# Kernel tuning notes

Measured on AMD Instinct MI355X. Metric: run time of the kernel, lower is better.

## Reference

```python
import jax, jax.numpy as jnp
import numpy as np

B, T, C, H, L, V = 4, 1024, 768, 12, 6, 32000
DH = C // H
EPS = 1e-5

def _ln(x, g, b):
    m = jnp.mean(x, axis=-1, keepdims=True)
    v = jnp.var(x, axis=-1, keepdims=True)
    return (x - m) * jax.lax.rsqrt(v + EPS) * g + b

def setup_inputs() -> dict:
    key = jax.random.key(0)
    ks = jax.random.split(key, 16)
    std = 0.02
    d = {
        'idx': jax.random.randint(ks[0], (B, T), 0, V),
        'tok_emb': jax.random.normal(ks[1], (V, C)) * std,
        'pos_emb': jnp.zeros((1, T, C)) + jax.random.normal(ks[2], (1, T, C)) * 0.01,
        'Wq': jax.random.normal(ks[3], (L, C, C)) * std, 'bq': jnp.zeros((L, C)),
        'Wk': jax.random.normal(ks[4], (L, C, C)) * std, 'bk': jnp.zeros((L, C)),
        'Wv': jax.random.normal(ks[5], (L, C, C)) * std, 'bv': jnp.zeros((L, C)),
        'Wo': jax.random.normal(ks[6], (L, C, C)) * std, 'bo': jnp.zeros((L, C)),
        'ln1_g': jnp.ones((L, C)), 'ln1_b': jnp.zeros((L, C)),
        'ln2_g': jnp.ones((L, C)), 'ln2_b': jnp.zeros((L, C)),
        'W1': jax.random.normal(ks[7], (L, C, 4 * C)) * std, 'b1': jnp.zeros((L, 4 * C)),
        'W2': jax.random.normal(ks[8], (L, 4 * C, C)) * std, 'b2': jnp.zeros((L, C)),
        'lnf_g': jnp.ones((C,)), 'lnf_b': jnp.zeros((C,)),
        'Whead': jax.random.normal(ks[9], (C, V)) * std,
    }
    return d

def _forward(idx, tok_emb, pos_emb, Wq, bq, Wk, bk, Wv, bv, Wo, bo,
             ln1_g, ln1_b, ln2_g, ln2_b, W1, b1, W2, b2, lnf_g, lnf_b, Whead):
    # pad-key mask: keys equal to vocab_size-1 are masked out (same for all queries)
    key_ok = (idx != V - 1)  # [B,T]
    x = tok_emb[idx] + pos_emb[:, :T, :]  # [B,T,C]
    for l in range(L):
        h = _ln(x, ln1_g[l], ln1_b[l])
        q = (h @ Wq[l] + bq[l]).reshape(B, T, H, DH)
        k = (h @ Wk[l] + bk[l]).reshape(B, T, H, DH)
        v = (h @ Wv[l] + bv[l]).reshape(B, T, H, DH)
        att = jnp.einsum('bqhd,bkhd->bhqk', q, k) * (1.0 / np.sqrt(DH))
        att = jnp.where(key_ok[:, None, None, :], att, -jnp.inf)
        att = jax.nn.softmax(att, axis=-1)
        y = jnp.einsum('bhqk,bkhd->bqhd', att, v).reshape(B, T, C)
        x = x + (y @ Wo[l] + bo[l])
        h2 = _ln(x, ln2_g[l], ln2_b[l])
        x = x + (jax.nn.gelu(h2 @ W1[l] + b1[l], approximate=False) @ W2[l] + b2[l])
    x = _ln(x, lnf_g, lnf_b)
    logits = x @ Whead  # [B,T,V]
    return logits

def reference(idx, tok_emb, pos_emb, Wq, bq, Wk, bk, Wv, bv, Wo, bo,
              ln1_g, ln1_b, ln2_g, ln2_b, W1, b1, W2, b2, lnf_g, lnf_b, Whead):
    logits = _forward(idx, tok_emb, pos_emb, Wq, bq, Wk, bk, Wv, bv, Wo, bo,
                      ln1_g, ln1_b, ln2_g, ln2_b, W1, b1, W2, b2, lnf_g, lnf_b, Whead)
    logsoftmax_logits = jax.nn.log_softmax(logits, axis=-1)
    softmax_logits = jax.nn.softmax(logits, axis=-1)
    seq_new_q = jnp.max(softmax_logits, axis=-1)
    seq_new = jnp.argmax(softmax_logits, axis=-1)
    return (seq_new, seq_new_q, logsoftmax_logits)
```

## Files before the change

kernel.cpp:

```cpp
#include <hip/hip_runtime.h>
#include <stdint.h>


#define B_ 4
#define T_ 1024
#define C_ 768
#define H_ 12
#define L_ 6
#define V_ 32000
#define CQ_ 2304
#define F_ 3072

typedef _Float16 f16;
typedef _Float16 f16x4 __attribute__((ext_vector_type(4)));
typedef _Float16 f16x8 __attribute__((ext_vector_type(8)));
typedef float f32x4 __attribute__((ext_vector_type(4)));

__device__ __forceinline__ f32x4 mfma16(f16x8 a, f16x8 b, f32x4 c) {
  return __builtin_amdgcn_mfma_f32_16x16x32_f16(a, b, c, 0, 0, 0);
}

__device__ __forceinline__ void gl_lds16(const void* g, void* l) {
  __builtin_amdgcn_global_load_lds((const __attribute__((address_space(1))) void*)g,
                                   (__attribute__((address_space(3))) void*)l, 16, 0, 0);
}

__global__ __launch_bounds__(256) void k_tsplit(const float* __restrict__ src,
    f16* __restrict__ dh, f16* __restrict__ dl, int K, int N,
    long long sS, long long dS)
{
  __shared__ float tile[64][68];
  src += (size_t)blockIdx.z * sS;
  dh += (size_t)blockIdx.z * dS;
  dl += (size_t)blockIdx.z * dS;
  const int t = threadIdx.x, tx = t & 15, ty = t >> 4;
  const int k0 = blockIdx.y * 64, n0 = blockIdx.x * 64;
#pragma unroll
  for (int rr = 0; rr < 4; rr++) {
    int row = ty + rr * 16;
    *(float4*)(&tile[row][tx * 4]) = *(const float4*)(src + (size_t)(k0 + row) * N + n0 + tx * 4);
  }
  __syncthreads();
#pragma unroll
  for (int rr = 0; rr < 4; rr++) {
    int nr = ty + rr * 16;
    f16x4 vh, vl;
#pragma unroll
    for (int j = 0; j < 4; j++) {
      float v = tile[tx * 4 + j][nr];
      f16 hv = (f16)v;
      vh[j] = hv;
      vl[j] = (f16)(v - (float)hv);
    }
    size_t o = (size_t)(n0 + nr) * K + k0 + tx * 4;
    *(f16x4*)(dh + o) = vh;
    *(f16x4*)(dl + o) = vl;
  }
}

__global__ __launch_bounds__(256) void k_bqkv(const float* __restrict__ bq, const float* __restrict__ bk,
    const float* __restrict__ bv, float* __restrict__ dst)
{
  int g = blockIdx.x * 256 + threadIdx.x;
  int lr = g / CQ_, j = g - lr * CQ_;
  float v;
  if (j < 768) v = bq[lr * 768 + j];
  else if (j < 1536) v = bk[lr * 768 + j - 768];
  else v = bv[lr * 768 + j - 1536];
  dst[g] = v;
}

__global__ __launch_bounds__(256) void k_embed(const int* __restrict__ idx, const float* __restrict__ tok,
    const float* __restrict__ pos, float* __restrict__ x)
{
  int g = blockIdx.x * 256 + threadIdx.x;
  int e = g * 4;
  int bt = e / C_;
  int c = e - bt * C_;
  int tt = bt & (T_ - 1);
  float4 a = *(const float4*)(tok + (size_t)idx[bt] * C_ + c);
  float4 p = *(const float4*)(pos + (size_t)tt * C_ + c);
  float4 o = {a.x + p.x, a.y + p.y, a.z + p.z, a.w + p.w};
  *(float4*)(x + e) = o;
}

__global__ __launch_bounds__(256) void k_ln(const float* __restrict__ x, const float* __restrict__ gg,
    const float* __restrict__ bb, f16* __restrict__ oh, f16* __restrict__ ol)
{
  __shared__ float red0[256], red1[256];
  const int row = blockIdx.x, t = threadIdx.x;
  const float* xr = x + (size_t)row * C_;
  float v0 = xr[t], v1 = xr[t + 256], v2 = xr[t + 512];
  red0[t] = v0 + v1 + v2;
  red1[t] = v0 * v0 + v1 * v1 + v2 * v2;
  __syncthreads();
  for (int off = 128; off > 0; off >>= 1) {
    if (t < off) { red0[t] += red0[t + off]; red1[t] += red1[t + off]; }
    __syncthreads();
  }
  const float mean = red0[0] * (1.f / C_);
  const float var = red1[0] * (1.f / C_) - mean * mean;
  const float rstd = rsqrtf(var + 1e-5f);
  const size_t o = (size_t)row * C_;
  float vv[3] = {v0, v1, v2};
#pragma unroll
  for (int i = 0; i < 3; i++) {
    int c = t + i * 256;
    float hv = (vv[i] - mean) * rstd * gg[c] + bb[c];
    f16 hh = (f16)hv;
    oh[o + c] = hh;
    ol[o + c] = (f16)(hv - (float)hh);
  }
}

template<int EPI>
__global__ __launch_bounds__(256, 2) void k_gemm(
    const f16* __restrict__ Ah, const f16* __restrict__ Al,
    const f16* __restrict__ Bh, const f16* __restrict__ Bl,
    const float* __restrict__ bias, const float* __restrict__ resid,
    float* __restrict__ outf, f16* __restrict__ outh, f16* __restrict__ outl,
    int M, int N, int K)
{
  __shared__ f16 sAh[128 * 32], sAl[128 * 32], sBh[128 * 32], sBl[128 * 32];
  const int t = threadIdx.x;
  const int l = t & 63, l15 = l & 15, quad = l >> 4;
  const int w = t >> 6;
  const int wm = (w >> 1) * 64, wn = (w & 1) * 64;
  const int m0 = blockIdx.y * 128, n0 = blockIdx.x * 128;
  const int r0 = t >> 2;
  const int c8 = (t & 3) * 8;

  f32x4 acc[4][4];
#pragma unroll
  for (int i = 0; i < 4; i++)
#pragma unroll
    for (int j = 0; j < 4; j++) acc[i][j] = (f32x4){0.f, 0.f, 0.f, 0.f};

  for (int k0 = 0; k0 < K; k0 += 32) {
    __syncthreads();
    const size_t ga0 = (size_t)(m0 + r0) * K + k0 + c8;
    const size_t ga1 = (size_t)(m0 + 64 + r0) * K + k0 + c8;
    const size_t gb0 = (size_t)(n0 + r0) * K + k0 + c8;
    const size_t gb1 = (size_t)(n0 + 64 + r0) * K + k0 + c8;
    gl_lds16(Ah + ga0, sAh + (size_t)t * 8);
    gl_lds16(Ah + ga1, sAh + (size_t)(256 + t) * 8);
    gl_lds16(Al + ga0, sAl + (size_t)t * 8);
    gl_lds16(Al + ga1, sAl + (size_t)(256 + t) * 8);
    gl_lds16(Bh + gb0, sBh + (size_t)t * 8);
    gl_lds16(Bh + gb1, sBh + (size_t)(256 + t) * 8);
    gl_lds16(Bl + gb0, sBl + (size_t)t * 8);
    gl_lds16(Bl + gb1, sBl + (size_t)(256 + t) * 8);
    __syncthreads();
    f16x8 fah[4], fal[4], fbh[4], fbl[4];
#pragma unroll
    for (int i = 0; i < 4; i++) {
      int ra = (wm + i * 16 + l15) * 32 + quad * 8;
      fah[i] = *(const f16x8*)(sAh + ra);
      fal[i] = *(const f16x8*)(sAl + ra);
    }
#pragma unroll
    for (int j = 0; j < 4; j++) {
      int rb = (wn + j * 16 + l15) * 32 + quad * 8;
      fbh[j] = *(const f16x8*)(sBh + rb);
      fbl[j] = *(const f16x8*)(sBl + rb);
    }
#pragma unroll
    for (int i = 0; i < 4; i++)
#pragma unroll
      for (int j = 0; j < 4; j++) {
        acc[i][j] = mfma16(fal[i], fbh[j], acc[i][j]);
        acc[i][j] = mfma16(fah[i], fbl[j], acc[i][j]);
        acc[i][j] = mfma16(fah[i], fbh[j], acc[i][j]);
      }
  }

#pragma unroll
  for (int j = 0; j < 4; j++) {
    int col = n0 + wn + j * 16 + l15;
    float bv = 0.f;
    if constexpr (EPI != 3) bv = bias[col];
#pragma unroll
    for (int i = 0; i < 4; i++) {
      int rowb = m0 + wm + i * 16 + quad * 4;
#pragma unroll
      for (int r = 0; r < 4; r++) {
        size_t o = (size_t)(rowb + r) * N + col;
        float v = acc[i][j][r] + bv;
        if constexpr (EPI == 1) v = 0.5f * v * (1.f + erff(v * 0.70710678118f));
        if constexpr (EPI == 0 || EPI == 1) {
          f16 hv = (f16)v;
          outh[o] = hv;
          outl[o] = (f16)(v - (float)hv);
        } else if constexpr (EPI == 2) {
          outf[o] = resid[o] + v;
        } else {
          outf[o] = v;
        }
      }
    }
  }
}

__global__ __launch_bounds__(256, 2) void k_attn(
    const f16* __restrict__ qh, const f16* __restrict__ ql,
    const int* __restrict__ idx, f16* __restrict__ yh, f16* __restrict__ yl)
{
  const int qt = blockIdx.x;
  const int hd = blockIdx.y;
  const int b = blockIdx.z;
  const int t = threadIdx.x, w = t >> 6, l = t & 63, l15 = l & 15, quad = l >> 4;

  __shared__ float maskadd[T_];
  __shared__ f16 Vth[64][40], Vtl[64][40];
  __shared__ f16 Pldsh[4][16][32], Pldsl[4][16][32];

  for (int i = t; i < T_; i += 256)
    maskadd[i] = (idx[b * T_ + i] == V_ - 1) ? -1e30f : 0.f;

  const size_t rq = (size_t)(b * T_ + qt * 64 + w * 16 + l15) * CQ_ + hd * 64 + quad * 8;
  f16x8 qAh = *(const f16x8*)(qh + rq);
  f16x8 qAl = *(const f16x8*)(ql + rq);
  f16x8 qBh = *(const f16x8*)(qh + rq + 32);
  f16x8 qBl = *(const f16x8*)(ql + rq + 32);

  f32x4 O[4];
  float m[4], lsum[4];
#pragma unroll
  for (int i = 0; i < 4; i++) { O[i] = (f32x4){0.f, 0.f, 0.f, 0.f}; m[i] = -1e30f; lsum[i] = 0.f; }

  for (int kc = 0; kc < T_; kc += 32) {
    __syncthreads();
    {
      int key = t >> 3, dg = (t & 7) * 8;
      size_t rv = (size_t)(b * T_ + kc + key) * CQ_ + 1536 + hd * 64 + dg;
      f16x8 vh = *(const f16x8*)(qh + rv);
      f16x8 vl = *(const f16x8*)(ql + rv);
#pragma unroll
      for (int j = 0; j < 8; j++) { Vth[dg + j][key] = vh[j]; Vtl[dg + j][key] = vl[j]; }
    }
    const size_t rk = (size_t)(b * T_ + kc + l15) * CQ_ + 768 + hd * 64 + quad * 8;
    f16x8 k0Ah = *(const f16x8*)(qh + rk);
    f16x8 k0Al = *(const f16x8*)(ql + rk);
    f16x8 k0Bh = *(const f16x8*)(qh + rk + 32);
    f16x8 k0Bl = *(const f16x8*)(ql + rk + 32);
    f16x8 k1Ah = *(const f16x8*)(qh + rk + 16 * CQ_);
    f16x8 k1Al = *(const f16x8*)(ql + rk + 16 * CQ_);
    f16x8 k1Bh = *(const f16x8*)(qh + rk + 16 * CQ_ + 32);
    f16x8 k1Bl = *(const f16x8*)(ql + rk + 16 * CQ_ + 32);

    f32x4 S0 = {0.f, 0.f, 0.f, 0.f}, S1 = {0.f, 0.f, 0.f, 0.f};
    S0 = mfma16(qAl, k0Ah, S0); S0 = mfma16(qAh, k0Al, S0); S0 = mfma16(qAh, k0Ah, S0);
    S0 = mfma16(qBl, k0Bh, S0); S0 = mfma16(qBh, k0Bl, S0); S0 = mfma16(qBh, k0Bh, S0);
    S1 = mfma16(qAl, k1Ah, S1); S1 = mfma16(qAh, k1Al, S1); S1 = mfma16(qAh, k1Ah, S1);
    S1 = mfma16(qBl, k1Bh, S1); S1 = mfma16(qBh, k1Bl, S1); S1 = mfma16(qBh, k1Bh, S1);

    const float mk0 = maskadd[kc + l15];
    const float mk1 = maskadd[kc + 16 + l15];
    float alpha[4];
#pragma unroll
    for (int r = 0; r < 4; r++) {
      float s0 = S0[r] * 0.125f + mk0;
      float s1 = S1[r] * 0.125f + mk1;
      float mx = fmaxf(s0, s1);
#pragma unroll
      for (int d = 1; d < 16; d <<= 1) mx = fmaxf(mx, __shfl_xor(mx, d));
      float mn = fmaxf(m[r], mx);
      float al = __expf(m[r] - mn);
      float p0 = __expf(s0 - mn);
      float p1 = __expf(s1 - mn);
      float rs = p0 + p1;
#pragma unroll
      for (int d = 1; d < 16; d <<= 1) rs += __shfl_xor(rs, d);
      lsum[r] = lsum[r] * al + rs;
      m[r] = mn;
      alpha[r] = al;
      f16 h0 = (f16)p0;
      Pldsh[w][quad * 4 + r][l15] = h0;
      Pldsl[w][quad * 4 + r][l15] = (f16)(p0 - (float)h0);
      f16 h1 = (f16)p1;
      Pldsh[w][quad * 4 + r][16 + l15] = h1;
      Pldsl[w][quad * 4 + r][16 + l15] = (f16)(p1 - (float)h1);
    }
#pragma unroll
    for (int dc = 0; dc < 4; dc++)
#pragma unroll
      for (int r = 0; r < 4; r++) O[dc][r] *= alpha[r];
    __syncthreads();
    f16x8 pfh = *(const f16x8*)(&Pldsh[w][l15][quad * 8]);
    f16x8 pfl = *(const f16x8*)(&Pldsl[w][l15][quad * 8]);
#pragma unroll
    for (int dc = 0; dc < 4; dc++) {
      f16x8 vfh = *(const f16x8*)(&Vth[dc * 16 + l15][quad * 8]);
      f16x8 vfl = *(const f16x8*)(&Vtl[dc * 16 + l15][quad * 8]);
      O[dc] = mfma16(pfl, vfh, O[dc]);
      O[dc] = mfma16(pfh, vfl, O[dc]);
      O[dc] = mfma16(pfh, vfh, O[dc]);
    }
  }

  float inv[4];
#pragma unroll
  for (int r = 0; r < 4; r++) inv[r] = 1.f / lsum[r];
  const int qr = qt * 64 + w * 16 + quad * 4;
#pragma unroll
  for (int r = 0; r < 4; r++) {
    size_t yo = (size_t)(b * T_ + qr + r) * C_ + hd * 64 + l15;
#pragma unroll
    for (int dc = 0; dc < 4; dc++) {
      float v = O[dc][r] * inv[r];
      f16 hv = (f16)v;
      yh[yo + dc * 16] = hv;
      yl[yo + dc * 16] = (f16)(v - (float)hv);
    }
  }
}

__global__ __launch_bounds__(256) void k_rowstat(const float* __restrict__ logits,
    float* __restrict__ logZ, float* __restrict__ out)
{
  __shared__ float smax[256], ssum[256];
  __shared__ int sidx[256];
  const int row = blockIdx.x, t = threadIdx.x;
  const float* lr = logits + (size_t)row * V_;
  float bm = -3e38f, bs = 0.f;
  int bi = 0;
  for (int c = t; c < V_; c += 256) {
    float v = lr[c];
    if (v > bm) { bs = bs * __expf(bm - v) + 1.f; bm = v; bi = c; }
    else bs += __expf(v - bm);
  }
  smax[t] = bm; ssum[t] = bs; sidx[t] = bi;
  __syncthreads();
  for (int off = 128; off > 0; off >>= 1) {
    if (t < off) {
      float m1 = smax[t], m2 = smax[t + off];
      float s1 = ssum[t], s2 = ssum[t + off];
      int i1 = sidx[t], i2 = sidx[t + off];
      float M = fmaxf(m1, m2);
      ssum[t] = s1 * __expf(m1 - M) + s2 * __expf(m2 - M);
      smax[t] = M;
      sidx[t] = (m2 > m1 || (m2 == m1 && i2 < i1)) ? i2 : i1;
    }
    __syncthreads();
  }
  if (t == 0) {
    float sum = ssum[0];
    logZ[row] = smax[0] + logf(sum);
    out[row] = (float)sidx[0];
    out[B_ * T_ + row] = 1.f / sum;
  }
}

__global__ __launch_bounds__(256) void k_lsm(const float* __restrict__ logits,
    const float* __restrict__ logZ, float* __restrict__ out2)
{
  const int row = blockIdx.y;
  const int c4 = blockIdx.x * 256 + threadIdx.x;
  if (c4 >= V_ / 4) return;
  const float lz = logZ[row];
  float4 v = *(const float4*)(logits + (size_t)row * V_ + c4 * 4);
  float4 o = {v.x - lz, v.y - lz, v.z - lz, v.w - lz};
  *(float4*)(out2 + (size_t)row * V_ + c4 * 4) = o;
}

extern "C" void kernel_launch(void* const* d_in, const int* in_sizes, int n_in,
                              void* d_out, int out_size, void* d_ws, size_t ws_size,
                              hipStream_t stream)
{
  (void)in_sizes; (void)n_in; (void)out_size; (void)ws_size;
  const int* idx = (const int*)d_in[0];
  const float* tok = (const float*)d_in[1];
  const float* pos = (const float*)d_in[2];
  const float* Wq = (const float*)d_in[3];
  const float* bq = (const float*)d_in[4];
  const float* Wk = (const float*)d_in[5];
  const float* bk = (const float*)d_in[6];
  const float* Wv = (const float*)d_in[7];
  const float* bv = (const float*)d_in[8];
  const float* Wo = (const float*)d_in[9];
  const float* bo = (const float*)d_in[10];
  const float* ln1g = (const float*)d_in[11];
  const float* ln1b = (const float*)d_in[12];
  const float* ln2g = (const float*)d_in[13];
  const float* ln2b = (const float*)d_in[14];
  const float* W1 = (const float*)d_in[15];
  const float* b1 = (const float*)d_in[16];
  const float* W2 = (const float*)d_in[17];
  const float* b2 = (const float*)d_in[18];
  const float* lnfg = (const float*)d_in[19];
  const float* lnfb = (const float*)d_in[20];
  const float* Wh = (const float*)d_in[21];

  char* ws = (char*)d_ws;
  size_t off = 0;
  auto alloc = [&](size_t bytes) -> char* {
    char* p = ws + off; off += (bytes + 255) & ~(size_t)255; return p;
  };
  float* x    = (float*)alloc((size_t)4096 * 768 * 4);
  f16* h_hi   = (f16*)alloc((size_t)4096 * 768 * 2);
  f16* h_lo   = (f16*)alloc((size_t)4096 * 768 * 2);
  f16* Wht_hi = (f16*)alloc((size_t)32000 * 768 * 2);
  f16* Wht_lo = (f16*)alloc((size_t)32000 * 768 * 2);
  float* logZ = (float*)alloc((size_t)4096 * 4);
  float* bqkv = (float*)alloc((size_t)6 * 2304 * 4);
  float* logits = (float*)(ws + off);
  f16* Wqkv_hi = (f16*)alloc((size_t)6 * 2304 * 768 * 2);
  f16* Wqkv_lo = (f16*)alloc((size_t)6 * 2304 * 768 * 2);
  f16* Wo_hi   = (f16*)alloc((size_t)6 * 768 * 768 * 2);
  f16* Wo_lo   = (f16*)alloc((size_t)6 * 768 * 768 * 2);
  f16* W1_hi   = (f16*)alloc((size_t)6 * 3072 * 768 * 2);
  f16* W1_lo   = (f16*)alloc((size_t)6 * 3072 * 768 * 2);
  f16* W2_hi   = (f16*)alloc((size_t)6 * 768 * 3072 * 2);
  f16* W2_lo   = (f16*)alloc((size_t)6 * 768 * 3072 * 2);
  f16* qkv_hi  = (f16*)alloc((size_t)4096 * 2304 * 2);
  f16* qkv_lo  = (f16*)alloc((size_t)4096 * 2304 * 2);
  f16* y_hi    = (f16*)alloc((size_t)4096 * 768 * 2);
  f16* y_lo    = (f16*)alloc((size_t)4096 * 768 * 2);
  f16* hid_hi  = (f16*)alloc((size_t)4096 * 3072 * 2);
  f16* hid_lo  = (f16*)alloc((size_t)4096 * 3072 * 2);

  float* out = (float*)d_out;
  float* out2 = out + 8192;

  k_tsplit<<<dim3(12, 12, 6), 256, 0, stream>>>(Wq, Wqkv_hi, Wqkv_lo, 768, 768, 589824LL, 1769472LL);
  k_tsplit<<<dim3(12, 12, 6), 256, 0, stream>>>(Wk, Wqkv_hi + 589824, Wqkv_lo + 589824, 768, 768, 589824LL, 1769472LL);
  k_tsplit<<<dim3(12, 12, 6), 256, 0, stream>>>(Wv, Wqkv_hi + 1179648, Wqkv_lo + 1179648, 768, 768, 589824LL, 1769472LL);
  k_tsplit<<<dim3(12, 12, 6), 256, 0, stream>>>(Wo, Wo_hi, Wo_lo, 768, 768, 589824LL, 589824LL);
  k_tsplit<<<dim3(48, 12, 6), 256, 0, stream>>>(W1, W1_hi, W1_lo, 768, 3072, 2359296LL, 2359296LL);
  k_tsplit<<<dim3(12, 48, 6), 256, 0, stream>>>(W2, W2_hi, W2_lo, 3072, 768, 2359296LL, 2359296LL);
  k_tsplit<<<dim3(500, 12, 1), 256, 0, stream>>>(Wh, Wht_hi, Wht_lo, 768, 32000, 0LL, 0LL);
  k_bqkv<<<54, 256, 0, stream>>>(bq, bk, bv, bqkv);
  k_embed<<<3072, 256, 0, stream>>>(idx, tok, pos, x);

  for (int lyr = 0; lyr < 6; lyr++) {
    k_ln<<<4096, 256, 0, stream>>>(x, ln1g + lyr * 768, ln1b + lyr * 768, h_hi, h_lo);
    k_gemm<0><<<dim3(18, 32), 256, 0, stream>>>(h_hi, h_lo,
        Wqkv_hi + (size_t)lyr * 1769472, Wqkv_lo + (size_t)lyr * 1769472,
        bqkv + lyr * 2304, nullptr, nullptr, qkv_hi, qkv_lo, 4096, 2304, 768);
    k_attn<<<dim3(16, 12, 4), 256, 0, stream>>>(qkv_hi, qkv_lo, idx, y_hi, y_lo);
    k_gemm<2><<<dim3(6, 32), 256, 0, stream>>>(y_hi, y_lo,
        Wo_hi + (size_t)lyr * 589824, Wo_lo + (size_t)lyr * 589824,
        bo + lyr * 768, x, x, nullptr, nullptr, 4096, 768, 768);
    k_ln<<<4096, 256, 0, stream>>>(x, ln2g + lyr * 768, ln2b + lyr * 768, h_hi, h_lo);
    k_gemm<1><<<dim3(24, 32), 256, 0, stream>>>(h_hi, h_lo,
        W1_hi + (size_t)lyr * 2359296, W1_lo + (size_t)lyr * 2359296,
        b1 + lyr * 3072, nullptr, nullptr, hid_hi, hid_lo, 4096, 3072, 768);
    k_gemm<2><<<dim3(6, 32), 256, 0, stream>>>(hid_hi, hid_lo,
        W2_hi + (size_t)lyr * 2359296, W2_lo + (size_t)lyr * 2359296,
        b2 + lyr * 768, x, x, nullptr, nullptr, 4096, 768, 3072);
  }
  k_ln<<<4096, 256, 0, stream>>>(x, lnfg, lnfb, h_hi, h_lo);
  k_gemm<3><<<dim3(250, 32), 256, 0, stream>>>(h_hi, h_lo, Wht_hi, Wht_lo,
      nullptr, nullptr, logits, nullptr, nullptr, 4096, 32000, 768);
  k_rowstat<<<4096, 256, 0, stream>>>(logits, logZ, out);
  k_lsm<<<dim3(32, 4096), 256, 0, stream>>>(logits, logZ, out2);
}
```

Before: 4.590 ms.

## Add larger-tile split-f16 GEMM with triple buffering for FFN1 and LM head

Adds a new GEMM kernel, k_hgemm, that uses 512 threads and 256x128 output tiles. It triple-buffers the K tiles in LDS through direct global-to-LDS loads, staggering the hi and lo halves around a barrier, and remaps block IDs across XCDs. Only the W1 projection and the large vocabulary head GEMM switch to it. The aim is more data reuse per tile and better overlap of loads with MFMA work. The cost is more LDS per block (about 144KB), which may limit occupancy, and 128-column tiles require N to be a multiple of 128, which holds for both 3072 and 32000.

```diff
diff --git a/kernel.cpp b/kernel.cpp
--- a/kernel.cpp
+++ b/kernel.cpp
@@ -193,6 +193,132 @@
           outl[o] = (f16)(v - (float)hv);
         } else if constexpr (EPI == 2) {
           outf[o] = resid[o] + v;
+        } else {
+          outf[o] = v;
+        }
+      }
+    }
+  }
+}
+
+template<int EPI>
+__global__ __launch_bounds__(512, 2) void k_hgemm(
+    const f16* __restrict__ Ah, const f16* __restrict__ Al,
+    const f16* __restrict__ Bh, const f16* __restrict__ Bl,
+    const float* __restrict__ bias,
+    float* __restrict__ outf, f16* __restrict__ outh, f16* __restrict__ outl,
+    int M, int N, int K)
+{
+  __shared__ __align__(16) f16 sm[3 * 24576];
+  const int t = threadIdx.x;
+  const int w = t >> 6, l15 = t & 15, quad = (t & 63) >> 4;
+  const int wm = (w >> 1) * 64, wn = (w & 1) * 64;
+
+  const int nwg = gridDim.x;
+  const int orig = blockIdx.x;
+  const int q = nwg >> 3, r = nwg & 7;
+  const int xcd = orig & 7, oj = orig >> 3;
+  const int wgid = (xcd < r ? xcd * (q + 1) : r * (q + 1) + (xcd - r) * q) + oj;
+  const int ntn = N >> 7;
+  const int m0 = (wgid / ntn) * 256;
+  const int n0 = (wgid % ntn) * 128;
+
+  const int swz8 = (quad ^ ((l15 >> 1) & 3)) * 8;
+  const int srow = t >> 2;
+  const int scol = ((t & 3) ^ ((t >> 3) & 3)) * 8;
+
+  auto stA = [&](const f16* __restrict__ src, int dbase, int k0) {
+    gl_lds16(src + (size_t)(m0 + srow) * K + k0 + scol, sm + dbase + t * 8);
+    gl_lds16(src + (size_t)(m0 + 128 + srow) * K + k0 + scol, sm + dbase + 4096 + t * 8);
+  };
+  auto stB = [&](const f16* __restrict__ src, int dbase, int k0) {
+    gl_lds16(src + (size_t)(n0 + srow) * K + k0 + scol, sm + dbase + t * 8);
+  };
+
+  f32x4 acc[4][4];
+#pragma unroll
+  for (int i = 0; i < 4; i++)
+#pragma unroll
+    for (int j = 0; j < 4; j++) acc[i][j] = (f32x4){0.f, 0.f, 0.f, 0.f};
+
+  stA(Ah, 0, 0); stB(Bh, 16384, 0); stA(Al, 8192, 0); stB(Bl, 20480, 0);
+  stA(Ah, 24576, 32); stB(Bh, 24576 + 16384, 32);
+  stA(Al, 24576 + 8192, 32); stB(Bl, 24576 + 20480, 32);
+
+  const int NT = K >> 5;
+  int sb = 0, wsb = 2 * 24576;
+  for (int tt = 0; tt < NT; ++tt) {
+    const int k2 = (tt + 2) << 5;
+    if (tt + 2 < NT) { stA(Ah, wsb, k2); stB(Bh, wsb + 16384, k2); }
+    if (tt + 2 < NT)      asm volatile("s_waitcnt vmcnt(9)" ::: "memory");
+    else if (tt + 1 < NT) asm volatile("s_waitcnt vmcnt(6)" ::: "memory");
+    else                  asm volatile("s_waitcnt vmcnt(0)" ::: "memory");
+    asm volatile("s_barrier" ::: "memory");
+    __builtin_amdgcn_sched_barrier(0);
+
+    f16x8 fah[4], fal[4];
+#pragma unroll
+    for (int i = 0; i < 4; i++) {
+      const int ra = sb + (wm + i * 16 + l15) * 32 + swz8;
+      fah[i] = *(const f16x8*)(sm + ra);
+      fal[i] = *(const f16x8*)(sm + 8192 + ra);
+    }
+    const int rb0 = sb + 16384 + (wn + l15) * 32 + swz8;
+    const int rb1 = rb0 + 16 * 32;
+    f16x8 fbh0 = *(const f16x8*)(sm + rb0), fbl0 = *(const f16x8*)(sm + 4096 + rb0);
+    f16x8 fbh1 = *(const f16x8*)(sm + rb1), fbl1 = *(const f16x8*)(sm + 4096 + rb1);
+    __builtin_amdgcn_s_setprio(1);
+#pragma unroll
+    for (int i = 0; i < 4; i++) {
+      acc[i][0] = mfma16(fal[i], fbh0, acc[i][0]);
+      acc[i][0] = mfma16(fah[i], fbl0, acc[i][0]);
+      acc[i][0] = mfma16(fah[i], fbh0, acc[i][0]);
+      acc[i][1] = mfma16(fal[i], fbh1, acc[i][1]);
+      acc[i][1] = mfma16(fah[i], fbl1, acc[i][1]);
+      acc[i][1] = mfma16(fah[i], fbh1, acc[i][1]);
+    }
+    __builtin_amdgcn_s_setprio(0);
+    __builtin_amdgcn_s_barrier();
+
+    if (tt + 2 < NT) { stA(Al, wsb + 8192, k2); stB(Bl, wsb + 20480, k2); }
+    const int rb2 = rb0 + 32 * 32;
+    const int rb3 = rb0 + 48 * 32;
+    f16x8 fbh2 = *(const f16x8*)(sm + rb2), fbl2 = *(const f16x8*)(sm + 4096 + rb2);
+    f16x8 fbh3 = *(const f16x8*)(sm + rb3), fbl3 = *(const f16x8*)(sm + 4096 + rb3);
+    __builtin_amdgcn_s_setprio(1);
+#pragma unroll
+    for (int i = 0; i < 4; i++) {
+      acc[i][2] = mfma16(fal[i], fbh2, acc[i][2]);
+      acc[i][2] = mfma16(fah[i], fbl2, acc[i][2]);
+      acc[i][2] = mfma16(fah[i], fbh2, acc[i][2]);
+      acc[i][3] = mfma16(fal[i], fbh3, acc[i][3]);
+      acc[i][3] = mfma16(fah[i], fbl3, acc[i][3]);
+      acc[i][3] = mfma16(fah[i], fbh3, acc[i][3]);
+    }
+    __builtin_amdgcn_s_setprio(0);
+    asm volatile("s_waitcnt lgkmcnt(0)" ::: "memory");
+    asm volatile("s_barrier" ::: "memory");
+    sb = (sb == 2 * 24576) ? 0 : sb + 24576;
+    wsb = (wsb == 2 * 24576) ? 0 : wsb + 24576;
+  }
+
+#pragma unroll
+  for (int j = 0; j < 4; j++) {
+    const int col = n0 + wn + j * 16 + l15;
+    float bv = 0.f;
+    if constexpr (EPI != 3) bv = bias[col];
+#pragma unroll
+    for (int i = 0; i < 4; i++) {
+      const int rowb = m0 + wm + i * 16 + quad * 4;
+#pragma unroll
+      for (int r4 = 0; r4 < 4; r4++) {
+        const size_t o = (size_t)(rowb + r4) * N + col;
+        float v = acc[i][j][r4] + bv;
+        if constexpr (EPI == 1) v = 0.5f * v * (1.f + erff(v * 0.70710678118f));
+        if constexpr (EPI == 0 || EPI == 1) {
+          f16 hv = (f16)v;
+          outh[o] = hv;
+          outl[o] = (f16)(v - (float)hv);
         } else {
           outf[o] = v;
         }
@@ -442,16 +568,16 @@
         Wo_hi + (size_t)lyr * 589824, Wo_lo + (size_t)lyr * 589824,
         bo + lyr * 768, x, x, nullptr, nullptr, 4096, 768, 768);
     k_ln<<<4096, 256, 0, stream>>>(x, ln2g + lyr * 768, ln2b + lyr * 768, h_hi, h_lo);
-    k_gemm<1><<<dim3(24, 32), 256, 0, stream>>>(h_hi, h_lo,
+    k_hgemm<1><<<dim3(384), 512, 0, stream>>>(h_hi, h_lo,
         W1_hi + (size_t)lyr * 2359296, W1_lo + (size_t)lyr * 2359296,
-        b1 + lyr * 3072, nullptr, nullptr, hid_hi, hid_lo, 4096, 3072, 768);
+        b1 + lyr * 3072, nullptr, hid_hi, hid_lo, 4096, 3072, 768);
     k_gemm<2><<<dim3(6, 32), 256, 0, stream>>>(hid_hi, hid_lo,
         W2_hi + (size_t)lyr * 2359296, W2_lo + (size_t)lyr * 2359296,
         b2 + lyr * 768, x, x, nullptr, nullptr, 4096, 768, 3072);
   }
   k_ln<<<4096, 256, 0, stream>>>(x, lnfg, lnfb, h_hi, h_lo);
-  k_gemm<3><<<dim3(250, 32), 256, 0, stream>>>(h_hi, h_lo, Wht_hi, Wht_lo,
-      nullptr, nullptr, logits, nullptr, nullptr, 4096, 32000, 768);
+  k_hgemm<3><<<dim3(4000), 512, 0, stream>>>(h_hi, h_lo, Wht_hi, Wht_lo,
+      nullptr, logits, nullptr, nullptr, 4096, 32000, 768);
   k_rowstat<<<4096, 256, 0, stream>>>(logits, logZ, out);
   k_lsm<<<dim3(32, 4096), 256, 0, stream>>>(logits, logZ, out2);
 }
```

After: 4.535 ms. No clear change (-1.2%).
